# Performance work log

Hardware: AMD Instinct MI355X
Metric: run time of the kernel (lower is better)

Reference implementation:

```python
import jax, jax.numpy as jnp
import numpy as np
from jax import lax


def _l2n(t, eps=1e-12):
    n = jnp.sqrt(jnp.sum(t * t, axis=-1, keepdims=True))
    return t / jnp.maximum(n, eps)


def _ln(t, w, b, eps=1e-5):
    mu = jnp.mean(t, -1, keepdims=True)
    var = jnp.var(t, -1, keepdims=True)
    return (t - mu) / jnp.sqrt(var + eps) * w + b


def _unfold3(x):
    # nn.Unfold(kernel_size=3, padding=1, stride=1): [B,C,H,W] -> [B,C,9,H*W]
    B, C, H, W = x.shape
    xp = jnp.pad(x, ((0, 0), (0, 0), (1, 1), (1, 1)))
    pat = jnp.stack([xp[:, :, i:i + H, j:j + W] for i in range(3) for j in range(3)], axis=2)
    return pat.reshape(B, C, 9, H * W)


def _forward(x, norm1_w, norm1_b, q_w, q_b, kv_w, kv_b, temperature, query_embedding,
             learnable_tokens, learnable_bias, sr_w, sr_b, pln_w, pln_b, proj_w, proj_b,
             norm2_w, norm2_b, fc1_w, fc1_b, dw_w, dw_b, fc2_w, fc2_b):
    B, C, H, W = x.shape
    nh = temperature.shape[0]
    d = C // nh
    N = H * W
    K = 9  # local_len = window_size**2
    # norm1 (WithBias LayerNorm over channel dim, channels-last)
    y = _ln(x.reshape(B, C, N).transpose(0, 2, 1), norm1_w, norm1_b)  # [B,N,C]
    # ---- AggregatedAttention ----
    q = (y @ q_w.T + q_b).reshape(B, N, nh, d).transpose(0, 2, 1, 3)  # [B,h,N,d]
    qn = _l2n(q)
    qs = (qn + query_embedding) * jax.nn.softplus(temperature)
    kv = y @ kv_w.T + kv_b  # [B,N,2C]
    k_loc = _l2n(kv[..., :C].reshape(B, N, nh, d)).reshape(B, N, C)
    kvl = jnp.concatenate([k_loc, kv[..., C:]], -1).transpose(0, 2, 1).reshape(B, 2 * C, H, W)
    pat = _unfold3(kvl).reshape(B, 2 * nh, d, K, N).transpose(0, 1, 4, 2, 3)  # [B,2h,N,d,K]
    k_l, v_l = pat[:, :nh], pat[:, nh:]
    attn_local = jnp.einsum('bhnd,bhndk->bhnk', qs, k_l)  # [B,h,N,K]
    # pooled branch; sr_ratio=1 so adaptive_avg_pool2d is identity
    y4 = y.transpose(0, 2, 1).reshape(B, C, H, W)
    xp = jax.nn.gelu(jnp.einsum('oc,bchw->bohw', sr_w, y4) + sr_b[:, None, None], approximate=False)
    xp = _ln(xp.reshape(B, C, N).transpose(0, 2, 1), pln_w, pln_b)  # [B,pool_len,C]
    kvp = (xp @ kv_w.T + kv_b).reshape(B, N, 2 * nh, d).transpose(0, 2, 1, 3)
    k_p = _l2n(kvp[:, :nh])
    v_p = kvp[:, nh:]
    attn_pool = jnp.einsum('bhnd,bhmd->bhnm', qs, k_p)  # [B,h,N,pool_len]
    attn = jax.nn.softmax(jnp.concatenate([attn_local, attn_pool], -1), axis=-1)
    a_l, a_p = attn[..., :K], attn[..., K:]
    w_l = jnp.einsum('bhnd,hdk->bhnk', qn, learnable_tokens) + learnable_bias + a_l
    x_local = jnp.einsum('bhnk,bhndk->bhnd', w_l, v_l)
    x_pool = jnp.einsum('bhnm,bhmd->bhnd', a_p, v_p)
    xo = (x_local + x_pool).transpose(0, 2, 1, 3).reshape(B, N, C)
    # proj then raw torch-style reshape [B,N,C] -> [B,C,H,W] (memory reinterpretation)
    xo = (xo @ proj_w.T + proj_b).reshape(B, C, H, W)
    x = x + xo
    # ---- ConvolutionalGLU MLP ----
    hf = dw_b.shape[0]
    y2 = _ln(x.reshape(B, C, N).transpose(0, 2, 1), norm2_w, norm2_b).transpose(0, 2, 1).reshape(B, C, H, W)
    f1 = jnp.einsum('oc,bchw->bohw', fc1_w, y2) + fc1_b[:, None, None]
    a, v = f1[:, :hf], f1[:, hf:]
    dw = lax.conv_general_dilated(a, dw_w, (1, 1), ((1, 1), (1, 1)),
                                  feature_group_count=hf,
                                  dimension_numbers=('NCHW', 'OIHW', 'NCHW')) + dw_b[:, None, None]
    g = jax.nn.gelu(dw, approximate=False) * v
    out = jnp.einsum('oc,bchw->bohw', fc2_w, g) + fc2_b[:, None, None]
    return x + out


def setup_inputs() -> dict:
    key = jax.random.key(0)
    B, C, H, W = 2, 128, 56, 56
    nh, d, K = 4, 32, 9
    hf = int(2 * int(C * 4.0) / 3)  # 341
    ks = iter(jax.random.split(key, 16))
    rn = lambda shape, s=0.02: jax.random.normal(next(ks), shape, jnp.float32) * s
    return {
        'x': jax.random.normal(next(ks), (B, C, H, W), jnp.float32),
        'norm1_w': jnp.ones((C,), jnp.float32), 'norm1_b': jnp.zeros((C,), jnp.float32),
        'q_w': rn((C, C)), 'q_b': jnp.zeros((C,), jnp.float32),
        'kv_w': rn((2 * C, C)), 'kv_b': jnp.zeros((2 * C,), jnp.float32),
        'temperature': jnp.full((nh, 1, 1), float(np.log(np.exp(1.0 / 0.24) - 1.0)), jnp.float32),
        'query_embedding': rn((nh, 1, d)),
        'learnable_tokens': rn((nh, d, K)),
        'learnable_bias': jnp.zeros((nh, 1, K), jnp.float32),
        'sr_w': rn((C, C)), 'sr_b': jnp.zeros((C,), jnp.float32),
        'pln_w': jnp.ones((C,), jnp.float32), 'pln_b': jnp.zeros((C,), jnp.float32),
        'proj_w': rn((C, C)), 'proj_b': jnp.zeros((C,), jnp.float32),
        'norm2_w': jnp.ones((C,), jnp.float32), 'norm2_b': jnp.zeros((C,), jnp.float32),
        'fc1_w': rn((2 * hf, C)), 'fc1_b': jnp.zeros((2 * hf,), jnp.float32),
        'dw_w': rn((hf, 1, 3, 3)), 'dw_b': jnp.zeros((hf,), jnp.float32),
        'fc2_w': rn((C, hf)), 'fc2_b': jnp.zeros((C,), jnp.float32),
    }


def reference(x, norm1_w, norm1_b, q_w, q_b, kv_w, kv_b, temperature, query_embedding,
              learnable_tokens, learnable_bias, sr_w, sr_b, pln_w, pln_b, proj_w, proj_b,
              norm2_w, norm2_b, fc1_w, fc1_b, dw_w, dw_b, fc2_w, fc2_b):
    return _forward(x, norm1_w, norm1_b, q_w, q_b, kv_w, kv_b, temperature, query_embedding,
                    learnable_tokens, learnable_bias, sr_w, sr_b, pln_w, pln_b, proj_w, proj_b,
                    norm2_w, norm2_b, fc1_w, fc1_b, dw_w, dw_b, fc2_w, fc2_b)
```

## Files before the change

### kernel.cpp

```cpp
#include <hip/hip_runtime.h>
#include <hip/hip_bf16.h>

typedef __hip_bfloat16 bf16;
typedef short s8v __attribute__((ext_vector_type(8)));
typedef short s4v __attribute__((ext_vector_type(4)));
typedef float f4v __attribute__((ext_vector_type(4)));

#define DEVI __device__ __forceinline__

DEVI float cvt(float x){ return x; }
DEVI float cvt(bf16 x){ return __bfloat162float(x); }

DEVI void stg(float* p, float v){ *p = v; }
DEVI void stg(bf16* p, float v){ *p = __float2bfloat16(v); }

DEVI float gelu_exact(float x){
  return 0.5f*x*(1.0f + erff(x*0.70710678118654752440f));
}

constexpr int B_ = 2, C_ = 128, H_ = 56, W_ = 56, N_ = 3136, NH_ = 4, D_ = 32, HF_ = 341;
constexpr int ROWS_ = B_*N_;
constexpr int KF2 = 352;
constexpr int GQ_ = NH_*B_*N_;
constexpr int FW = 512;
constexpr int KSP = 4;

template<typename TX, typename TY, bool PLANES>
__global__ __launch_bounds__(256)
void ln_kernel(const TX* __restrict__ x, long xstr, const float* __restrict__ w,
               const float* __restrict__ bia, TY* __restrict__ y)
{
  int gid = blockIdx.x*4 + (threadIdx.x>>6);
  int lane = threadIdx.x & 63;
  int b = gid / N_, n = gid % N_;
  float v0, v1;
  if (PLANES){
    v0 = cvt(x[((long)b*C_ + lane     )*N_ + n]);
    v1 = cvt(x[((long)b*C_ + lane + 64)*N_ + n]);
  } else {
    v0 = cvt(x[(long)gid*xstr + lane     ]);
    v1 = cvt(x[(long)gid*xstr + lane + 64]);
  }
  float s = v0+v1, ss = v0*v0 + v1*v1;
  #pragma unroll
  for (int o=32;o>0;o>>=1){ s += __shfl_xor(s,o); ss += __shfl_xor(ss,o); }
  float mu  = s*(1.0f/128.0f);
  float var = fmaxf(ss*(1.0f/128.0f) - mu*mu, 0.f);
  float inv = rsqrtf(var + 1e-5f);
  stg(&y[(long)gid*C_ + lane     ], (v0-mu)*inv*w[lane     ] + bia[lane     ]);
  stg(&y[(long)gid*C_ + lane + 64], (v1-mu)*inv*w[lane + 64] + bia[lane + 64]);
}

__global__ __launch_bounds__(256)
void convw_kernel(const float* __restrict__ q_w, const float* __restrict__ kv_w,
                  const float* __restrict__ sr_w, const float* __restrict__ proj_w,
                  const float* __restrict__ fc1_w, const float* __restrict__ fc2_w,
                  const float* __restrict__ q_b, const float* __restrict__ kv_b,
                  const float* __restrict__ sr_b,
                  bf16* __restrict__ out, float* __restrict__ bias_out)
{
  int t = blockIdx.x*256 + threadIdx.x;
  if (t >= 214272){
    int i = t - 214272;
    if (i < 512){
      float bv = (i < 128) ? q_b[i] : (i < 384) ? kv_b[i-128] : sr_b[i-384];
      bias_out[i] = bv;
    }
    return;
  }
  float v;
  if      (t <  16384) v = q_w[t];
  else if (t <  49152) v = kv_w[t-16384];
  else if (t <  65536) v = sr_w[t-49152];
  else if (t <  81920) v = proj_w[t-65536];
  else if (t < 169216) v = fc1_w[t-81920];
  else {
    int i = t - 169216; int m = i / KF2, kp = i % KF2;
    v = (kp < HF_) ? fc2_w[m*HF_ + kp] : 0.f;
  }
  out[t] = __float2bfloat16(v);
}

template<int KT, int MODE, typename TC>
__global__ __launch_bounds__(256)
void gemm_mfma(const bf16* __restrict__ A, const bf16* __restrict__ B,
               const float* __restrict__ bias, const float* __restrict__ res,
               TC* __restrict__ Cm, int M, int Nn,
               long sA, long sB, long sC, long sR,
               const float* __restrict__ qe, const float* __restrict__ temp,
               bf16* __restrict__ aux0, bf16* __restrict__ aux1)
{
  A  += (long)blockIdx.z * sA;
  B  += (long)blockIdx.z * sB;
  Cm += (long)blockIdx.z * sC;
  if (res) res += (long)blockIdx.z * sR;
  int lane = threadIdx.x & 63, w = threadIdx.x >> 6;
  int m = lane & 15, quad = lane >> 4;
  int n0 = blockIdx.x*64, m0 = blockIdx.y*64;
  int arow = m0 + w*16 + m;
  if (arow >= M) arow = M-1;
  const bf16* ap = A + (long)arow*KT + quad*8;
  const bf16* bp = B + (long)(n0 + m)*KT + quad*8;
  f4v acc[4];
  #pragma unroll
  for (int s=0;s<4;s++) acc[s] = (f4v){0.f,0.f,0.f,0.f};
  #pragma unroll
  for (int k0 = 0; k0 < KT; k0 += 32){
    s8v af = *(const s8v*)(ap + k0);
    #pragma unroll
    for (int s=0;s<4;s++){
      s8v bf = *(const s8v*)(bp + (long)s*16*KT + k0);
      acc[s] = __builtin_amdgcn_mfma_f32_16x16x32_bf16(af, bf, acc[s], 0, 0, 0);
    }
  }
  if ((MODE==6 || MODE==7) && blockIdx.x < 2){
    int hA = blockIdx.x*2, hB = hA+1;
    float spA = 0.f, spB = 0.f;
    if (MODE==6){ spA = log1pf(expf(temp[hA])); spB = log1pf(expf(temp[hB])); }
    #pragma unroll
    for (int r=0;r<4;r++){
      float v4[4];
      #pragma unroll
      for (int s=0;s<4;s++) v4[s] = acc[s][r] + bias[n0 + s*16 + m];
      float ssA = v4[0]*v4[0] + v4[1]*v4[1];
      float ssB = v4[2]*v4[2] + v4[3]*v4[3];
      #pragma unroll
      for (int off=1; off<16; off<<=1){
        ssA += __shfl_xor(ssA, off);
        ssB += __shfl_xor(ssB, off);
      }
      float invA = 1.f/fmaxf(sqrtf(ssA), 1e-12f);
      float invB = 1.f/fmaxf(sqrtf(ssB), 1e-12f);
      int gm = m0 + w*16 + quad*4 + r;
      int b = gm / N_, n = gm % N_;
      #pragma unroll
      for (int s=0;s<4;s++){
        int h = (s<2) ? hA : hB;
        int d = (s&1)*16 + m;
        float v = v4[s] * ((s<2) ? invA : invB);
        if (MODE==6) v = (v + qe[h*D_ + d]) * ((s<2) ? spA : spB);
        aux0[((long)(b*NH_+h)*N_ + n)*D_ + d] = __float2bfloat16(v);
      }
    }
    return;
  }
  if (MODE==7){
    int gm0 = m0 + w*16 + quad*4;
    int b = gm0 / N_, nb = gm0 % N_;
    #pragma unroll
    for (int s=0;s<4;s++){
      int h = (blockIdx.x-2)*2 + (s>>1);
      int d = (s&1)*16 + m;
      bf16 p4[4];
      #pragma unroll
      for (int r=0;r<4;r++) p4[r] = __float2bfloat16(acc[s][r] + bias[n0 + s*16 + m]);
      *(s4v*)(aux1 + ((long)(b*NH_+h)*D_ + d)*N_ + nb) = *(const s4v*)p4;
    }
    return;
  }
  #pragma unroll
  for (int s=0;s<4;s++){
    int gn = n0 + s*16 + m;
    #pragma unroll
    for (int r=0;r<4;r++){
      int gm = m0 + w*16 + quad*4 + r;
      if (gm >= M) continue;
      float v = acc[s][r];
      if (MODE==1 || MODE==4 || MODE==6) v += bias[gn];
      else                               v += bias[gm];
      if (MODE==6 && gn >= 384) v = gelu_exact(v);
      if (MODE==4 || MODE==5) v += res[(long)gm*Nn + gn];
      stg(&Cm[(long)gm*Nn + gn], v);
    }
  }
}

__global__ __launch_bounds__(256)
void attn_part_kernel(const bf16* __restrict__ qs_, const bf16* __restrict__ kp_,
                      const bf16* __restrict__ vp_,
                      bf16* __restrict__ Op, float* __restrict__ Lp)
{
  int bh = blockIdx.y;
  int z  = blockIdx.z;
  int lane = threadIdx.x & 63;
  int w    = threadIdx.x >> 6;
  int m    = lane & 15, quad = lane >> 4;
  int base = blockIdx.x*256 + w*16;
  __shared__ float sm[4][2304];
  bf16*  Pl   = (bf16*)sm[w];
  float* Olds = sm[w];

  s8v af[4]; bool hasQ[4];
  #pragma unroll
  for (int ch=0; ch<4; ch++){
    int qq = base + ch*64;
    hasQ[ch] = (qq < N_);
    af[ch] = *(const s8v*)(qs_ + ((long)bh*N_ + (hasQ[ch] ? qq : base) + m)*D_ + quad*8);
  }
  const bf16* kpb = kp_ + (long)bh*N_*D_;
  const bf16* vpb = vp_ + (long)bh*D_*N_;
  f4v o0[4], o1[4];
  float l[4][4];
  #pragma unroll
  for (int ch=0; ch<4; ch++){
    o0[ch] = (f4v){0.f,0.f,0.f,0.f}; o1[ch] = (f4v){0.f,0.f,0.f,0.f};
    #pragma unroll
    for (int r=0;r<4;r++) l[ch][r] = 0.f;
  }

  int tlo = z*768, thi = (z==KSP-1) ? N_ : tlo + 768;
  for (int t0 = tlo; t0 < thi; t0 += 64){
    s8v kf[4], vf[4];
    #pragma unroll
    for (int s=0;s<4;s++)
      kf[s] = *(const s8v*)(kpb + (long)(t0 + s*16 + m)*D_ + quad*8);
    vf[0] = *(const s8v*)(vpb + (long)(m     )*N_ + t0      + quad*8);
    vf[1] = *(const s8v*)(vpb + (long)(16 + m)*N_ + t0      + quad*8);
    vf[2] = *(const s8v*)(vpb + (long)(m     )*N_ + t0 + 32 + quad*8);
    vf[3] = *(const s8v*)(vpb + (long)(16 + m)*N_ + t0 + 32 + quad*8);
    #pragma unroll
    for (int s = 0; s < 4; s++){
      #pragma unroll
      for (int ch=0; ch<4; ch++){
        f4v c = {0.f,0.f,0.f,0.f};
        c = __builtin_amdgcn_mfma_f32_16x16x32_bf16(af[ch], kf[s], c, 0, 0, 0);
        #pragma unroll
        for (int r=0;r<4;r++){
          float e = __expf(c[r] - 8.f);
          l[ch][r] += e;
          Pl[ch*1152 + (quad*4+r)*72 + s*16 + m] = __float2bfloat16(e);
        }
      }
    }
    #pragma unroll
    for (int c2=0;c2<2;c2++){
      #pragma unroll
      for (int ch=0; ch<4; ch++){
        s8v pa = *(const s8v*)(Pl + ch*1152 + m*72 + c2*32 + quad*8);
        o0[ch] = __builtin_amdgcn_mfma_f32_16x16x32_bf16(pa, vf[c2*2  ], o0[ch], 0, 0, 0);
        o1[ch] = __builtin_amdgcn_mfma_f32_16x16x32_bf16(pa, vf[c2*2+1], o1[ch], 0, 0, 0);
      }
    }
  }
  #pragma unroll
  for (int ch=0; ch<4; ch++){
    if (!hasQ[ch]) continue;
    float lr[4] = {l[ch][0], l[ch][1], l[ch][2], l[ch][3]};
    #pragma unroll
    for (int off=1; off<16; off<<=1)
      #pragma unroll
      for (int r=0;r<4;r++) lr[r] += __shfl_xor(lr[r], off);
    #pragma unroll
    for (int r=0;r<4;r++){
      Olds[(quad*4+r)*36 + m     ] = o0[ch][r];
      Olds[(quad*4+r)*36 + 16 + m] = o1[ch][r];
    }
    if (m == 0){
      #pragma unroll
      for (int r=0;r<4;r++) Olds[576 + quad*4 + r] = lr[r];
    }
    long gq = (long)bh*N_ + base + ch*64 + m;
    f4v ov0 = *(const f4v*)(Olds + m*36 + quad*8);
    f4v ov1 = *(const f4v*)(Olds + m*36 + quad*8 + 4);
    bf16 o8[8];
    #pragma unroll
    for (int j=0;j<4;j++){ o8[j] = __float2bfloat16(ov0[j]); o8[4+j] = __float2bfloat16(ov1[j]); }
    *(s8v*)(Op + ((long)z*GQ_ + gq)*32 + quad*8) = *(const s8v*)o8;
    if (quad == 0) Lp[(long)z*GQ_ + gq] = Olds[576 + m];
  }
}

__global__ __launch_bounds__(256)
void attn_combine_kernel(const bf16* __restrict__ Op, const float* __restrict__ Lp,
                         const bf16* __restrict__ qs_, const bf16* __restrict__ fused,
                         const float* __restrict__ qe, const float* __restrict__ temp,
                         const float* __restrict__ tokens, const float* __restrict__ tbias,
                         bf16* __restrict__ xo)
{
  int gq = blockIdx.x*256 + threadIdx.x;
  int n = gq % N_; int bh = gq / N_; int h = bh & 3; int b = bh >> 2;
  float L = 0.f;
  float out[32];
  #pragma unroll
  for (int d=0;d<32;d++) out[d] = 0.f;
  #pragma unroll
  for (int z=0; z<KSP; z++){
    L += Lp[(long)z*GQ_ + gq];
    const bf16* oz = Op + ((long)z*GQ_ + gq)*32;
    #pragma unroll
    for (int d=0;d<32;d++) out[d] += cvt(oz[d]);
  }
  const bf16* qrow = qs_ + (long)gq*D_;
  float q[32];
  #pragma unroll
  for (int d=0;d<32;d++) q[d] = cvt(qrow[d]);
  int hy = n / W_, wx = n % W_;
  const bf16* kvb = fused + (long)b*N_*FW + 128 + h*D_;
  float sl[9];
  #pragma unroll
  for (int k=0;k<9;k++){
    int di = k/3-1, dj = k%3-1;
    int yy = hy+di, xx = wx+dj;
    float s = 0.f;
    if (yy>=0 && yy<H_ && xx>=0 && xx<W_){
      long nn2 = (long)(yy*W_+xx)*FW;
      float dot = 0.f, ss = 0.f;
      #pragma unroll
      for (int d=0;d<32;d++){
        float kk = cvt(kvb[nn2 + d]);
        dot = fmaf(q[d], kk, dot);
        ss  = fmaf(kk, kk, ss);
      }
      s = dot / fmaxf(sqrtf(ss), 1e-12f);
    }
    sl[k] = s;
  }
  #pragma unroll
  for (int k=0;k<9;k++) L += __expf(sl[k] - 8.f);
  float invL = 1.f/L;
  #pragma unroll
  for (int d=0;d<32;d++) out[d] *= invL;
  float sp = log1pf(expf(temp[h]));
  float invsp = 1.f/sp;
  float qn[32];
  #pragma unroll
  for (int d=0;d<32;d++) qn[d] = q[d]*invsp - qe[h*D_+d];
  #pragma unroll
  for (int k=0;k<9;k++){
    float tok = 0.f;
    #pragma unroll
    for (int d=0;d<32;d++) tok = fmaf(qn[d], tokens[(h*D_+d)*9+k], tok);
    float wl = tok + tbias[h*9+k] + __expf(sl[k] - 8.f)*invL;
    int di = k/3-1, dj = k%3-1;
    int yy = hy+di, xx = wx+dj;
    if (yy>=0 && yy<H_ && xx>=0 && xx<W_){
      long nn2 = (long)(yy*W_+xx)*FW;
      #pragma unroll
      for (int d=0;d<32;d++) out[d] = fmaf(wl, cvt(kvb[nn2 + 128 + d]), out[d]);
    }
  }
  bf16* op = xo + ((long)(b*N_ + n))*C_ + h*D_;
  #pragma unroll
  for (int d=0;d<32;d++) stg(&op[d], out[d]);
}

__global__ __launch_bounds__(256)
void dwconv_kernel(const bf16* __restrict__ f1, const float* __restrict__ dww,
                   const float* __restrict__ dwb, bf16* __restrict__ g)
{
  int t = blockIdx.x*256 + threadIdx.x;
  if (t >= B_*N_*44) return;
  int b = t / (N_*44); int r = t - b*(N_*44);
  int n = r % N_, cg = r / N_;
  f1 += (long)b*2*HF_*N_;
  g  += (long)b*N_*KF2;
  int c0 = cg*8;
  int hy = n / W_, wx = n % W_;
  bf16 o8[8];
  #pragma unroll
  for (int j=0;j<8;j++){
    int c = c0 + j;
    float val = 0.f;
    if (c < HF_){
      const bf16* ap = f1 + (long)c*N_;
      float s = dwb[c];
      #pragma unroll
      for (int di=-1; di<=1; di++)
        #pragma unroll
        for (int dj=-1; dj<=1; dj++){
          int yy = hy+di, xx = wx+dj;
          if (yy>=0 && yy<H_ && xx>=0 && xx<W_)
            s = fmaf(dww[c*9 + (di+1)*3 + (dj+1)], cvt(ap[yy*W_+xx]), s);
        }
      val = gelu_exact(s) * cvt(f1[(long)(HF_+c)*N_ + n]);
    }
    o8[j] = __float2bfloat16(val);
  }
  *(s8v*)(g + (long)n*KF2 + c0) = *(const s8v*)o8;
}

extern "C" void kernel_launch(void* const* d_in, const int* in_sizes, int n_in,
                              void* d_out, int out_size, void* d_ws, size_t ws_size,
                              hipStream_t stream)
{
  (void)in_sizes; (void)n_in; (void)out_size; (void)ws_size;
  const float* x_in      = (const float*)d_in[0];
  const float* norm1_w   = (const float*)d_in[1];
  const float* norm1_b   = (const float*)d_in[2];
  const float* q_w       = (const float*)d_in[3];
  const float* q_b       = (const float*)d_in[4];
  const float* kv_w      = (const float*)d_in[5];
  const float* kv_b      = (const float*)d_in[6];
  const float* temp      = (const float*)d_in[7];
  const float* qe        = (const float*)d_in[8];
  const float* tokens    = (const float*)d_in[9];
  const float* tbias     = (const float*)d_in[10];
  const float* sr_w      = (const float*)d_in[11];
  const float* sr_b      = (const float*)d_in[12];
  const float* pln_w     = (const float*)d_in[13];
  const float* pln_b     = (const float*)d_in[14];
  const float* proj_w    = (const float*)d_in[15];
  const float* proj_b    = (const float*)d_in[16];
  const float* norm2_w   = (const float*)d_in[17];
  const float* norm2_b   = (const float*)d_in[18];
  const float* fc1_w     = (const float*)d_in[19];
  const float* fc1_b     = (const float*)d_in[20];
  const float* dw_w      = (const float*)d_in[21];
  const float* dw_b      = (const float*)d_in[22];
  const float* fc2_w     = (const float*)d_in[23];
  const float* fc2_b     = (const float*)d_in[24];

  char* w8 = (char*)d_ws;
  bf16*  fused   = (bf16*)(w8 + 0);
  float* x2      = (float*)(w8 + 0);
  bf16*  y2      = (bf16*)(w8 + 3211264);
  bf16*  f1b     = (bf16*)(w8 + 4816896);
  bf16*  qs      = (bf16*)(w8 + 6422528);
  bf16*  xp      = (bf16*)(w8 + 8028160);
  bf16*  k_p     = (bf16*)(w8 + 9633792);
  bf16*  v_p     = (bf16*)(w8 + 11239424);
  bf16*  Opart   = (bf16*)(w8 + 13045056);
  bf16*  g_rows  = (bf16*)(w8 + 19467584);
  bf16*  wbase   = (bf16*)(w8 + 23883072);
  float* fbias   = (float*)(w8 + 24311616);
  bf16*  y       = f1b;
  bf16*  xo      = (bf16*)d_out;
  float* Lpart   = (float*)((char*)d_out + 1605632);
  bf16*  proj_wb = wbase + 65536;
  bf16*  fc1_wb  = wbase + 81920;
  bf16*  fc2_wb  = wbase + 169216;

  convw_kernel<<<(214784+255)/256, 256, 0, stream>>>(
      q_w, kv_w, sr_w, proj_w, fc1_w, fc2_w, q_b, kv_b, sr_b, wbase, fbias);
  ln_kernel<float, bf16, true><<<ROWS_/4, 256, 0, stream>>>(x_in, 0, norm1_w, norm1_b, y);
  gemm_mfma<128, 6, bf16><<<dim3(8,98), 256, 0, stream>>>(
      y, wbase, fbias, nullptr, fused, ROWS_, FW, 0,0,0,0, qe, temp, qs, nullptr);
  ln_kernel<bf16, bf16, false><<<ROWS_/4, 256, 0, stream>>>(fused + 384, FW, pln_w, pln_b, xp);
  gemm_mfma<128, 7, bf16><<<dim3(4,98), 256, 0, stream>>>(
      xp, wbase + 16384, kv_b, nullptr, (bf16*)nullptr, ROWS_, 256, 0,0,0,0,
      nullptr, nullptr, k_p, v_p);
  attn_part_kernel<<<dim3(13,8,KSP), 256, 0, stream>>>(qs, k_p, v_p, Opart, Lpart);
  attn_combine_kernel<<<GQ_/256, 256, 0, stream>>>(Opart, Lpart, qs, fused,
                                                   qe, temp, tokens, tbias, xo);
  gemm_mfma<128, 4, float><<<dim3(2,98), 256, 0, stream>>>(
      xo, proj_wb, proj_b, x_in, x2, ROWS_, 128, 0,0,0,0, nullptr, nullptr, nullptr, nullptr);
  ln_kernel<float, bf16, true><<<ROWS_/4, 256, 0, stream>>>(x2, 0, norm2_w, norm2_b, y2);
  gemm_mfma<128, 3, bf16><<<dim3(49,11,B_), 256, 0, stream>>>(
      fc1_wb, y2, fc1_b, nullptr, f1b, 2*HF_, N_,
      0, (long)N_*C_, (long)2*HF_*N_, 0, nullptr, nullptr, nullptr, nullptr);
  dwconv_kernel<<<(B_*N_*44+255)/256, 256, 0, stream>>>(f1b, dw_w, dw_b, g_rows);
  gemm_mfma<KF2, 5, float><<<dim3(49,2,B_), 256, 0, stream>>>(
      fc2_wb, g_rows, fc2_b, x2, (float*)d_out, C_, N_,
      0, (long)N_*KF2, (long)C_*N_, (long)C_*N_, nullptr, nullptr, nullptr, nullptr);
}
```

Measured before the change: 264.9 us.

## Use exp2 with log2e-prescaled queries, transposed MFMA, and doubled key splits

Pre-scales the softplus temperature by log2(e) so the attention kernel can use a raw exp2 with the -8 offset folded into the MFMA accumulator init. It also swaps the MFMA operands so each lane holds scores for one query row. That allows a single row-sum accumulator, a cheaper shuffle reduction and packed 4-element P stores. Key splits double to 8 (384 keys each) for more parallelism, with workspace offsets moved to fit the larger partial buffer. The combine kernel rescales q by ln2 to undo the prescale for the local branch. The costs are more partials to combine and a risk of inconsistent scaling in branches not shown.

```diff
diff --git a/kernel.cpp b/kernel.cpp
--- a/kernel.cpp
+++ b/kernel.cpp
@@ -23,7 +23,10 @@
 constexpr int KF2 = 352;
 constexpr int GQ_ = NH_*B_*N_;
 constexpr int FW = 512;
-constexpr int KSP = 4;
+constexpr int KSP = 8;
+constexpr int SPLIT = 384;
+constexpr float LOG2E = 1.4426950408889634f;
+constexpr float E8L2  = 11.541560327111707f;
 
 template<typename TX, typename TY, bool PLANES>
 __global__ __launch_bounds__(256)
@@ -116,7 +119,10 @@
   if ((MODE==6 || MODE==7) && blockIdx.x < 2){
     int hA = blockIdx.x*2, hB = hA+1;
     float spA = 0.f, spB = 0.f;
-    if (MODE==6){ spA = log1pf(expf(temp[hA])); spB = log1pf(expf(temp[hB])); }
+    if (MODE==6){
+      spA = log1pf(expf(temp[hA])) * LOG2E;
+      spB = log1pf(expf(temp[hB])) * LOG2E;
+    }
     #pragma unroll
     for (int r=0;r<4;r++){
       float v4[4];
@@ -200,15 +206,14 @@
   const bf16* kpb = kp_ + (long)bh*N_*D_;
   const bf16* vpb = vp_ + (long)bh*D_*N_;
   f4v o0[4], o1[4];
-  float l[4][4];
+  float l[4];
   #pragma unroll
   for (int ch=0; ch<4; ch++){
     o0[ch] = (f4v){0.f,0.f,0.f,0.f}; o1[ch] = (f4v){0.f,0.f,0.f,0.f};
-    #pragma unroll
-    for (int r=0;r<4;r++) l[ch][r] = 0.f;
-  }
-
-  int tlo = z*768, thi = (z==KSP-1) ? N_ : tlo + 768;
+    l[ch] = 0.f;
+  }
+
+  int tlo = z*SPLIT, thi = (z==KSP-1) ? N_ : tlo + SPLIT;
   for (int t0 = tlo; t0 < thi; t0 += 64){
     s8v kf[4], vf[4];
     #pragma unroll
@@ -222,14 +227,17 @@
     for (int s = 0; s < 4; s++){
       #pragma unroll
       for (int ch=0; ch<4; ch++){
-        f4v c = {0.f,0.f,0.f,0.f};
-        c = __builtin_amdgcn_mfma_f32_16x16x32_bf16(af[ch], kf[s], c, 0, 0, 0);
-        #pragma unroll
-        for (int r=0;r<4;r++){
-          float e = __expf(c[r] - 8.f);
-          l[ch][r] += e;
-          Pl[ch*1152 + (quad*4+r)*72 + s*16 + m] = __float2bfloat16(e);
-        }
+        f4v c = {-E8L2, -E8L2, -E8L2, -E8L2};
+        c = __builtin_amdgcn_mfma_f32_16x16x32_bf16(kf[s], af[ch], c, 0, 0, 0);
+        bf16 p4[4];
+        float e0 = __builtin_amdgcn_exp2f(c[0]);
+        float e1 = __builtin_amdgcn_exp2f(c[1]);
+        float e2 = __builtin_amdgcn_exp2f(c[2]);
+        float e3 = __builtin_amdgcn_exp2f(c[3]);
+        l[ch] += (e0+e1) + (e2+e3);
+        p4[0] = __float2bfloat16(e0); p4[1] = __float2bfloat16(e1);
+        p4[2] = __float2bfloat16(e2); p4[3] = __float2bfloat16(e3);
+        *(s4v*)(Pl + ch*1152 + m*72 + s*16 + quad*4) = *(const s4v*)p4;
       }
     }
     #pragma unroll
@@ -245,19 +253,13 @@
   #pragma unroll
   for (int ch=0; ch<4; ch++){
     if (!hasQ[ch]) continue;
-    float lr[4] = {l[ch][0], l[ch][1], l[ch][2], l[ch][3]};
-    #pragma unroll
-    for (int off=1; off<16; off<<=1)
-      #pragma unroll
-      for (int r=0;r<4;r++) lr[r] += __shfl_xor(lr[r], off);
+    float lr = l[ch];
+    lr += __shfl_xor(lr, 16);
+    lr += __shfl_xor(lr, 32);
     #pragma unroll
     for (int r=0;r<4;r++){
       Olds[(quad*4+r)*36 + m     ] = o0[ch][r];
       Olds[(quad*4+r)*36 + 16 + m] = o1[ch][r];
-    }
-    if (m == 0){
-      #pragma unroll
-      for (int r=0;r<4;r++) Olds[576 + quad*4 + r] = lr[r];
     }
     long gq = (long)bh*N_ + base + ch*64 + m;
     f4v ov0 = *(const f4v*)(Olds + m*36 + quad*8);
@@ -266,7 +268,7 @@
     #pragma unroll
     for (int j=0;j<4;j++){ o8[j] = __float2bfloat16(ov0[j]); o8[4+j] = __float2bfloat16(ov1[j]); }
     *(s8v*)(Op + ((long)z*GQ_ + gq)*32 + quad*8) = *(const s8v*)o8;
-    if (quad == 0) Lp[(long)z*GQ_ + gq] = Olds[576 + m];
+    if (quad == 0) Lp[(long)z*GQ_ + gq] = lr;
   }
 }
 
@@ -293,7 +295,7 @@
   const bf16* qrow = qs_ + (long)gq*D_;
   float q[32];
   #pragma unroll
-  for (int d=0;d<32;d++) q[d] = cvt(qrow[d]);
+  for (int d=0;d<32;d++) q[d] = cvt(qrow[d]) * 0.6931471805599453f;
   int hy = n / W_, wx = n % W_;
   const bf16* kvb = fused + (long)b*N_*FW + 128 + h*D_;
   float sl[9];
@@ -420,9 +422,9 @@
   bf16*  k_p     = (bf16*)(w8 + 9633792);
   bf16*  v_p     = (bf16*)(w8 + 11239424);
   bf16*  Opart   = (bf16*)(w8 + 13045056);
-  bf16*  g_rows  = (bf16*)(w8 + 19467584);
-  bf16*  wbase   = (bf16*)(w8 + 23883072);
-  float* fbias   = (float*)(w8 + 24311616);
+  bf16*  g_rows  = (bf16*)(w8 + 25890112);
+  bf16*  wbase   = (bf16*)(w8 + 30305600);
+  float* fbias   = (float*)(w8 + 30734144);
   bf16*  y       = f1b;
   bf16*  xo      = (bf16*)d_out;
   float* Lpart   = (float*)((char*)d_out + 1605632);
```

Result: faster. 251.7 us (-5.0%).
